# Optimization experiments

Hardware: AMD Instinct MI355X
Metric: run time of the kernel (lower is better)

The kernel has to match this reference:

```python
import jax, jax.numpy as jnp
import numpy as np

N, D, V = 2048, 64, 2048


def setup_inputs() -> dict:
    key = jax.random.key(0)
    k_ids, k_emb, k_tree, k_map = jax.random.split(key, 4)
    language_ids = jax.random.randint(k_ids, (N,), 0, V)
    language_embeddings = jax.random.normal(k_emb, (N, D), dtype=jnp.float32)
    # symmetric distance tables, mimicking the symmetric try/except dict lookup
    t = jax.random.uniform(k_tree, (V, V), dtype=jnp.float32)
    tree_dist = (t + t.T) * 0.5
    m = jax.random.uniform(k_map, (V, V), dtype=jnp.float32)
    map_dist = (m + m.T) * 0.5
    return {
        "language_ids": language_ids,
        "language_embeddings": language_embeddings,
        "tree_dist": tree_dist,
        "map_dist": map_dist,
    }


def reference(language_ids, language_embeddings, tree_dist, map_dist):
    # pairwise mean-L1 distance between embeddings: [N, N]
    emb_dist = jnp.mean(
        jnp.abs(language_embeddings[:, None, :] - language_embeddings[None, :, :]),
        axis=-1,
    )
    # largest_value_map_dist as computed in __init__
    largest = jnp.max(map_dist)
    ii = language_ids[:, None]  # [N, 1]
    jj = language_ids[None, :]  # [1, N]
    metric = (tree_dist[ii, jj] + map_dist[ii, jj] / largest) * 0.5  # [N, N]
    # pairs with equal language ids are skipped in the original loop
    mask = (ii != jj).astype(emb_dist.dtype)
    per_pair = jnp.abs(emb_dist - metric) * mask
    return jnp.sum(per_pair) / jnp.sum(mask)
```

## Files before the change

kernel.cpp:

```cpp
#include <hip/hip_runtime.h>
#include <hip/hip_bf16.h>

#define NL 2048
#define DE 64
#define VV 2048
#define BT 64
#define NT (NL / BT)
#define NBLK (NT * (NT + 1) / 2)
#define STT 68


__global__ __launch_bounds__(1024) void prep_kernel(const int* __restrict__ ids,
                                                    const float4* __restrict__ m4,
                                                    float* __restrict__ pmax,
                                                    int* __restrict__ perm,
                                                    int* __restrict__ sids) {
    const int t = threadIdx.x;
    const int lane = t & 63, wave = t >> 6;
    const int b = blockIdx.x;

    if (b < 256) {
        const float4* p = m4 + (size_t)b * 4096;
        const float4 x0 = p[t], x1 = p[t + 1024], x2 = p[t + 2048], x3 = p[t + 3072];
        float v = fmaxf(fmaxf(fmaxf(x0.x, x0.y), fmaxf(x0.z, x0.w)),
                        fmaxf(fmaxf(x1.x, x1.y), fmaxf(x1.z, x1.w)));
        v = fmaxf(v, fmaxf(fmaxf(x2.x, x2.y), fmaxf(x2.z, x2.w)));
        v = fmaxf(v, fmaxf(fmaxf(x3.x, x3.y), fmaxf(x3.z, x3.w)));
        #pragma unroll
        for (int o = 32; o > 0; o >>= 1)
            v = fmaxf(v, __shfl_down(v, o));
        __shared__ float wl[16];
        if (lane == 0) wl[wave] = v;
        __syncthreads();
        if (t == 0) {
            float m = wl[0];
            #pragma unroll
            for (int i = 1; i < 16; ++i) m = fmaxf(m, wl[i]);
            pmax[b] = m;
        }
    } else {
        __shared__ unsigned hist[VV];
        __shared__ unsigned offs[VV];
        __shared__ unsigned wtot[16];
        __shared__ unsigned wexc[16];
        hist[2 * t] = 0u; hist[2 * t + 1] = 0u;
        __syncthreads();
        const int id0 = ids[2 * t], id1 = ids[2 * t + 1];
        atomicAdd(&hist[id0], 1u);
        atomicAdd(&hist[id1], 1u);
        __syncthreads();
        const unsigned h0 = hist[2 * t], h1 = hist[2 * t + 1];
        const unsigned s = h0 + h1;
        unsigned ps = s;
        #pragma unroll
        for (int o = 1; o < 64; o <<= 1) {
            unsigned u = __shfl_up(ps, o);
            if (lane >= o) ps += u;
        }
        if (lane == 63) wtot[wave] = ps;
        __syncthreads();
        if (wave == 0 && lane < 16) {
            unsigned v = wtot[lane];
            unsigned pv = v;
            #pragma unroll
            for (int o = 1; o < 16; o <<= 1) {
                unsigned u = __shfl_up(pv, o);
                if (lane >= o) pv += u;
            }
            wexc[lane] = pv - v;
        }
        __syncthreads();
        const unsigned ex = wexc[wave] + ps - s;
        offs[2 * t]     = ex;
        offs[2 * t + 1] = ex + h0;
        __syncthreads();
        unsigned p0 = atomicAdd(&offs[id0], 1u);
        perm[p0] = 2 * t;     sids[p0] = id0;
        unsigned p1 = atomicAdd(&offs[id1], 1u);
        perm[p1] = 2 * t + 1; sids[p1] = id1;
    }
}

__global__ __launch_bounds__(256) void loss_kernel(
    const float* __restrict__ emb,
    const float* __restrict__ tree, const float* __restrict__ mapd,
    const int* __restrict__ perm, const int* __restrict__ sids,
    const float* __restrict__ pmax,
    float* __restrict__ psum, unsigned* __restrict__ pcnt)
{
    const int t = threadIdx.x;

    const int L = blockIdx.x;
    int bi = (int)((65.0f - sqrtf(4225.0f - 8.0f * (float)L)) * 0.5f);
    if (bi > NT - 1) bi = NT - 1;
    if (bi < 0) bi = 0;
    while (NT * bi - bi * (bi - 1) / 2 > L) --bi;
    while (NT * (bi + 1) - (bi + 1) * bi / 2 <= L) ++bi;
    const int bj = bi + (L - (NT * bi - bi * (bi - 1) / 2));

    __shared__ __align__(16) float Eit[DE][STT];
    __shared__ __align__(16) float Ejt[DE][STT];
    __shared__ int idi[BT];
    __shared__ int idj[BT];
    __shared__ float wm[4];

    float pv = pmax[t];

    {
        const int r  = t & 63;
        const int c0 = (t >> 6) << 4;
        const int gi = perm[bi * BT + r];
        const int gj = perm[bj * BT + r];
        const float4* pa = (const float4*)(emb + (size_t)gi * DE + c0);
        const float4* pb = (const float4*)(emb + (size_t)gj * DE + c0);
        float4 a0 = pa[0], a1 = pa[1], a2 = pa[2], a3 = pa[3];
        float4 b0 = pb[0], b1 = pb[1], b2 = pb[2], b3 = pb[3];
        Eit[c0 + 0][r]  = a0.x; Eit[c0 + 1][r]  = a0.y; Eit[c0 + 2][r]  = a0.z; Eit[c0 + 3][r]  = a0.w;
        Eit[c0 + 4][r]  = a1.x; Eit[c0 + 5][r]  = a1.y; Eit[c0 + 6][r]  = a1.z; Eit[c0 + 7][r]  = a1.w;
        Eit[c0 + 8][r]  = a2.x; Eit[c0 + 9][r]  = a2.y; Eit[c0 + 10][r] = a2.z; Eit[c0 + 11][r] = a2.w;
        Eit[c0 + 12][r] = a3.x; Eit[c0 + 13][r] = a3.y; Eit[c0 + 14][r] = a3.z; Eit[c0 + 15][r] = a3.w;
        Ejt[c0 + 0][r]  = b0.x; Ejt[c0 + 1][r]  = b0.y; Ejt[c0 + 2][r]  = b0.z; Ejt[c0 + 3][r]  = b0.w;
        Ejt[c0 + 4][r]  = b1.x; Ejt[c0 + 5][r]  = b1.y; Ejt[c0 + 6][r]  = b1.z; Ejt[c0 + 7][r]  = b1.w;
        Ejt[c0 + 8][r]  = b2.x; Ejt[c0 + 9][r]  = b2.y; Ejt[c0 + 10][r] = b2.z; Ejt[c0 + 11][r] = b2.w;
        Ejt[c0 + 12][r] = b3.x; Ejt[c0 + 13][r] = b3.y; Ejt[c0 + 14][r] = b3.z; Ejt[c0 + 15][r] = b3.w;
        if (t < BT)          idi[t] = sids[bi * BT + t];
        else if (t < 2 * BT) idj[t - BT] = sids[bj * BT + (t - BT)];
    }
    #pragma unroll
    for (int o = 32; o > 0; o >>= 1)
        pv = fmaxf(pv, __shfl_down(pv, o));
    if ((t & 63) == 0) wm[t >> 6] = pv;
    __syncthreads();

    const float inv = 1.0f / fmaxf(fmaxf(wm[0], wm[1]), fmaxf(wm[2], wm[3]));

    const int i0 = (t >> 4) * 4;
    const int j0 = (t & 15) * 4;

    int ia[4], ja[4];
    #pragma unroll
    for (int s = 0; s < 4; ++s) { ia[s] = idi[i0 + s]; ja[s] = idj[j0 + s]; }
    float tg[4][4], mg[4][4];
    #pragma unroll
    for (int s = 0; s < 4; ++s)
        #pragma unroll
        for (int c = 0; c < 4; ++c) {
            const int off = ia[s] * VV + ja[c];
            tg[s][c] = tree[off];
            mg[s][c] = mapd[off];
        }

    float acc[4][4];
    #pragma unroll
    for (int s = 0; s < 4; ++s)
        #pragma unroll
        for (int c = 0; c < 4; ++c) acc[s][c] = 0.0f;

    #pragma unroll 2
    for (int k = 0; k < 16; ++k) {
        #pragma unroll
        for (int q = 0; q < 4; ++q) {
            const int d = 4 * k + q;
            const float4 a = *(const float4*)&Eit[d][i0];
            const float4 b = *(const float4*)&Ejt[d][j0];
            acc[0][0] += fabsf(a.x - b.x); acc[0][1] += fabsf(a.x - b.y);
            acc[0][2] += fabsf(a.x - b.z); acc[0][3] += fabsf(a.x - b.w);
            acc[1][0] += fabsf(a.y - b.x); acc[1][1] += fabsf(a.y - b.y);
            acc[1][2] += fabsf(a.y - b.z); acc[1][3] += fabsf(a.y - b.w);
            acc[2][0] += fabsf(a.z - b.x); acc[2][1] += fabsf(a.z - b.y);
            acc[2][2] += fabsf(a.z - b.z); acc[2][3] += fabsf(a.z - b.w);
            acc[3][0] += fabsf(a.w - b.x); acc[3][1] += fabsf(a.w - b.y);
            acc[3][2] += fabsf(a.w - b.z); acc[3][3] += fabsf(a.w - b.w);
        }
    }

    float pp = 0.0f;
    unsigned cnt = 0;
    #pragma unroll
    for (int s = 0; s < 4; ++s)
        #pragma unroll
        for (int c = 0; c < 4; ++c) {
            const float metric = (tg[s][c] + mg[s][c] * inv) * 0.5f;
            if (ia[s] != ja[c]) {
                pp += fabsf(acc[s][c] * (1.0f / (float)DE) - metric);
                cnt += 1u;
            }
        }

    #pragma unroll
    for (int o = 32; o > 0; o >>= 1) {
        pp  += __shfl_down(pp, o);
        cnt += __shfl_down(cnt, o);
    }
    __shared__ float    wsum_l[4];
    __shared__ unsigned wcnt_l[4];
    if ((t & 63) == 0) { wsum_l[t >> 6] = pp; wcnt_l[t >> 6] = cnt; }
    __syncthreads();
    if (t == 0) {
        const float    w = (bi == bj) ? 1.0f : 2.0f;
        const unsigned u = (bi == bj) ? 1u : 2u;
        psum[L] = (wsum_l[0] + wsum_l[1] + wsum_l[2] + wsum_l[3]) * w;
        pcnt[L] = (wcnt_l[0] + wcnt_l[1] + wcnt_l[2] + wcnt_l[3]) * u;
    }
}

__global__ __launch_bounds__(1024) void finalize_kernel(const float* __restrict__ psum,
                                                        const unsigned* __restrict__ pcnt,
                                                        float* __restrict__ out) {
    const int t = threadIdx.x;
    const int lane = t & 63, wave = t >> 6;
    double s = 0.0;
    unsigned c = 0;
    if (t < NBLK) { s = (double)psum[t]; c = pcnt[t]; }
    #pragma unroll
    for (int o = 32; o > 0; o >>= 1) {
        s += __shfl_down(s, o);
        c += __shfl_down(c, o);
    }
    __shared__ double   sl[16];
    __shared__ unsigned cl[16];
    if (lane == 0) { sl[wave] = s; cl[wave] = c; }
    __syncthreads();
    if (t == 0) {
        double   S = sl[0];
        unsigned C = cl[0];
        #pragma unroll
        for (int i = 1; i < 16; ++i) { S += sl[i]; C += cl[i]; }
        out[0] = (float)(S / (double)C);
    }
}

extern "C" void kernel_launch(void* const* d_in, const int* in_sizes, int n_in,
                              void* d_out, int out_size, void* d_ws, size_t ws_size,
                              hipStream_t stream) {
    const int*   ids  = (const int*)d_in[0];
    const float* emb  = (const float*)d_in[1];
    const float* tree = (const float*)d_in[2];
    const float* mapd = (const float*)d_in[3];
    float* out = (float*)d_out;

    float*    pmax = (float*)d_ws;
    int*      perm = (int*)((char*)d_ws + 1024);
    int*      sids = (int*)((char*)d_ws + 9216);
    float*    psum = (float*)((char*)d_ws + 17408);
    unsigned* pcnt = (unsigned*)((char*)d_ws + 19520);

    prep_kernel<<<257, 1024, 0, stream>>>(ids, (const float4*)mapd, pmax, perm, sids);

    loss_kernel<<<NBLK, 256, 0, stream>>>(emb, tree, mapd, perm, sids, pmax, psum, pcnt);

    finalize_kernel<<<1, 1024, 0, stream>>>(psum, pcnt, out);
}
```

Measured before the change: 103.2 us.

## Split loss tiles into 64x32 blocks with exact upper-triangle masking

Changes the pairwise tile shape from 64x64 to 64x32, doubling the number of blocks, and remaps the triangular block index accordingly. Diagonal-straddling tiles now use a per-element position check with doubled weight instead of whole-block weighting. Finalize loops over more partials. This aims for better load balance and occupancy, at the cost of less register reuse per thread (4x2 outputs) and more shared-memory reads per arithmetic op.

```diff
diff --git a/kernel.cpp b/kernel.cpp
--- a/kernel.cpp
+++ b/kernel.cpp
@@ -4,10 +4,13 @@
 #define NL 2048
 #define DE 64
 #define VV 2048
-#define BT 64
-#define NT (NL / BT)
-#define NBLK (NT * (NT + 1) / 2)
-#define STT 68
+#define BI 64
+#define BJ 32
+#define NTI (NL / BI)
+#define NTJ (NL / BJ)
+#define NBLK 1056
+#define STI 68
+#define STJ 36
 
 
 __global__ __launch_bounds__(1024) void prep_kernel(const int* __restrict__ ids,
@@ -91,17 +94,17 @@
     const int t = threadIdx.x;
 
     const int L = blockIdx.x;
-    int bi = (int)((65.0f - sqrtf(4225.0f - 8.0f * (float)L)) * 0.5f);
-    if (bi > NT - 1) bi = NT - 1;
+    int bi = (int)((65.0f - sqrtf(4225.0f - 4.0f * (float)L)) * 0.5f);
+    if (bi > NTI - 1) bi = NTI - 1;
     if (bi < 0) bi = 0;
-    while (NT * bi - bi * (bi - 1) / 2 > L) --bi;
-    while (NT * (bi + 1) - (bi + 1) * bi / 2 <= L) ++bi;
-    const int bj = bi + (L - (NT * bi - bi * (bi - 1) / 2));
-
-    __shared__ __align__(16) float Eit[DE][STT];
-    __shared__ __align__(16) float Ejt[DE][STT];
-    __shared__ int idi[BT];
-    __shared__ int idj[BT];
+    while (65 * bi - bi * bi > L) --bi;
+    while (65 * (bi + 1) - (bi + 1) * (bi + 1) <= L) ++bi;
+    const int bj = 2 * bi + (L - (65 * bi - bi * bi));
+
+    __shared__ __align__(16) float Eit[DE][STI];
+    __shared__ __align__(16) float Ejt[DE][STJ];
+    __shared__ int idi[BI];
+    __shared__ int idj[BJ];
     __shared__ float wm[4];
 
     float pv = pmax[t];
@@ -109,22 +112,24 @@
     {
         const int r  = t & 63;
         const int c0 = (t >> 6) << 4;
-        const int gi = perm[bi * BT + r];
-        const int gj = perm[bj * BT + r];
+        const int gi = perm[bi * BI + r];
         const float4* pa = (const float4*)(emb + (size_t)gi * DE + c0);
-        const float4* pb = (const float4*)(emb + (size_t)gj * DE + c0);
         float4 a0 = pa[0], a1 = pa[1], a2 = pa[2], a3 = pa[3];
-        float4 b0 = pb[0], b1 = pb[1], b2 = pb[2], b3 = pb[3];
         Eit[c0 + 0][r]  = a0.x; Eit[c0 + 1][r]  = a0.y; Eit[c0 + 2][r]  = a0.z; Eit[c0 + 3][r]  = a0.w;
         Eit[c0 + 4][r]  = a1.x; Eit[c0 + 5][r]  = a1.y; Eit[c0 + 6][r]  = a1.z; Eit[c0 + 7][r]  = a1.w;
         Eit[c0 + 8][r]  = a2.x; Eit[c0 + 9][r]  = a2.y; Eit[c0 + 10][r] = a2.z; Eit[c0 + 11][r] = a2.w;
         Eit[c0 + 12][r] = a3.x; Eit[c0 + 13][r] = a3.y; Eit[c0 + 14][r] = a3.z; Eit[c0 + 15][r] = a3.w;
-        Ejt[c0 + 0][r]  = b0.x; Ejt[c0 + 1][r]  = b0.y; Ejt[c0 + 2][r]  = b0.z; Ejt[c0 + 3][r]  = b0.w;
-        Ejt[c0 + 4][r]  = b1.x; Ejt[c0 + 5][r]  = b1.y; Ejt[c0 + 6][r]  = b1.z; Ejt[c0 + 7][r]  = b1.w;
-        Ejt[c0 + 8][r]  = b2.x; Ejt[c0 + 9][r]  = b2.y; Ejt[c0 + 10][r] = b2.z; Ejt[c0 + 11][r] = b2.w;
-        Ejt[c0 + 12][r] = b3.x; Ejt[c0 + 13][r] = b3.y; Ejt[c0 + 14][r] = b3.z; Ejt[c0 + 15][r] = b3.w;
-        if (t < BT)          idi[t] = sids[bi * BT + t];
-        else if (t < 2 * BT) idj[t - BT] = sids[bj * BT + (t - BT)];
+
+        const int rj  = t & 31;
+        const int cj0 = (t >> 5) << 3;
+        const int gj = perm[bj * BJ + rj];
+        const float4* pb = (const float4*)(emb + (size_t)gj * DE + cj0);
+        float4 b0 = pb[0], b1 = pb[1];
+        Ejt[cj0 + 0][rj] = b0.x; Ejt[cj0 + 1][rj] = b0.y; Ejt[cj0 + 2][rj] = b0.z; Ejt[cj0 + 3][rj] = b0.w;
+        Ejt[cj0 + 4][rj] = b1.x; Ejt[cj0 + 5][rj] = b1.y; Ejt[cj0 + 6][rj] = b1.z; Ejt[cj0 + 7][rj] = b1.w;
+
+        if (t < BI)            idi[t] = sids[bi * BI + t];
+        else if (t < BI + BJ)  idj[t - BI] = sids[bj * BJ + (t - BI)];
     }
     #pragma unroll
     for (int o = 32; o > 0; o >>= 1)
@@ -135,26 +140,26 @@
     const float inv = 1.0f / fmaxf(fmaxf(wm[0], wm[1]), fmaxf(wm[2], wm[3]));
 
     const int i0 = (t >> 4) * 4;
-    const int j0 = (t & 15) * 4;
-
-    int ia[4], ja[4];
-    #pragma unroll
-    for (int s = 0; s < 4; ++s) { ia[s] = idi[i0 + s]; ja[s] = idj[j0 + s]; }
-    float tg[4][4], mg[4][4];
+    const int j0 = (t & 15) * 2;
+
+    int ia[4], ja[2];
+    #pragma unroll
+    for (int s = 0; s < 4; ++s) ia[s] = idi[i0 + s];
+    #pragma unroll
+    for (int c = 0; c < 2; ++c) ja[c] = idj[j0 + c];
+    float tg[4][2], mg[4][2];
     #pragma unroll
     for (int s = 0; s < 4; ++s)
         #pragma unroll
-        for (int c = 0; c < 4; ++c) {
+        for (int c = 0; c < 2; ++c) {
             const int off = ia[s] * VV + ja[c];
             tg[s][c] = tree[off];
             mg[s][c] = mapd[off];
         }
 
-    float acc[4][4];
-    #pragma unroll
-    for (int s = 0; s < 4; ++s)
-        #pragma unroll
-        for (int c = 0; c < 4; ++c) acc[s][c] = 0.0f;
+    float acc[4][2];
+    #pragma unroll
+    for (int s = 0; s < 4; ++s) { acc[s][0] = 0.0f; acc[s][1] = 0.0f; }
 
     #pragma unroll 2
     for (int k = 0; k < 16; ++k) {
@@ -162,30 +167,29 @@
         for (int q = 0; q < 4; ++q) {
             const int d = 4 * k + q;
             const float4 a = *(const float4*)&Eit[d][i0];
-            const float4 b = *(const float4*)&Ejt[d][j0];
+            const float2 b = *(const float2*)&Ejt[d][j0];
             acc[0][0] += fabsf(a.x - b.x); acc[0][1] += fabsf(a.x - b.y);
-            acc[0][2] += fabsf(a.x - b.z); acc[0][3] += fabsf(a.x - b.w);
             acc[1][0] += fabsf(a.y - b.x); acc[1][1] += fabsf(a.y - b.y);
-            acc[1][2] += fabsf(a.y - b.z); acc[1][3] += fabsf(a.y - b.w);
             acc[2][0] += fabsf(a.z - b.x); acc[2][1] += fabsf(a.z - b.y);
-            acc[2][2] += fabsf(a.z - b.z); acc[2][3] += fabsf(a.z - b.w);
             acc[3][0] += fabsf(a.w - b.x); acc[3][1] += fabsf(a.w - b.y);
-            acc[3][2] += fabsf(a.w - b.z); acc[3][3] += fabsf(a.w - b.w);
         }
     }
 
     float pp = 0.0f;
     unsigned cnt = 0;
     #pragma unroll
-    for (int s = 0; s < 4; ++s)
-        #pragma unroll
-        for (int c = 0; c < 4; ++c) {
-            const float metric = (tg[s][c] + mg[s][c] * inv) * 0.5f;
-            if (ia[s] != ja[c]) {
-                pp += fabsf(acc[s][c] * (1.0f / (float)DE) - metric);
-                cnt += 1u;
+    for (int s = 0; s < 4; ++s) {
+        const int posi = bi * BI + i0 + s;
+        #pragma unroll
+        for (int c = 0; c < 2; ++c) {
+            const int posj = bj * BJ + j0 + c;
+            if (posi < posj && ia[s] != ja[c]) {
+                const float metric = (tg[s][c] + mg[s][c] * inv) * 0.5f;
+                pp += 2.0f * fabsf(acc[s][c] * (1.0f / (float)DE) - metric);
+                cnt += 2u;
             }
         }
+    }
 
     #pragma unroll
     for (int o = 32; o > 0; o >>= 1) {
@@ -197,10 +201,8 @@
     if ((t & 63) == 0) { wsum_l[t >> 6] = pp; wcnt_l[t >> 6] = cnt; }
     __syncthreads();
     if (t == 0) {
-        const float    w = (bi == bj) ? 1.0f : 2.0f;
-        const unsigned u = (bi == bj) ? 1u : 2u;
-        psum[L] = (wsum_l[0] + wsum_l[1] + wsum_l[2] + wsum_l[3]) * w;
-        pcnt[L] = (wcnt_l[0] + wcnt_l[1] + wcnt_l[2] + wcnt_l[3]) * u;
+        psum[L] = wsum_l[0] + wsum_l[1] + wsum_l[2] + wsum_l[3];
+        pcnt[L] = wcnt_l[0] + wcnt_l[1] + wcnt_l[2] + wcnt_l[3];
     }
 }
 
@@ -211,7 +213,7 @@
     const int lane = t & 63, wave = t >> 6;
     double s = 0.0;
     unsigned c = 0;
-    if (t < NBLK) { s = (double)psum[t]; c = pcnt[t]; }
+    for (int i = t; i < NBLK; i += 1024) { s += (double)psum[i]; c += pcnt[i]; }
     #pragma unroll
     for (int o = 32; o > 0; o >>= 1) {
         s += __shfl_down(s, o);
@@ -243,7 +245,7 @@
     int*      perm = (int*)((char*)d_ws + 1024);
     int*      sids = (int*)((char*)d_ws + 9216);
     float*    psum = (float*)((char*)d_ws + 17408);
-    unsigned* pcnt = (unsigned*)((char*)d_ws + 19520);
+    unsigned* pcnt = (unsigned*)((char*)d_ws + 21632);
 
     prep_kernel<<<257, 1024, 0, stream>>>(ids, (const float4*)mapd, pmax, perm, sids);
 
```

After: 100.5 us. 1.03x faster.
